# Performance work log

Measured on AMD Instinct MI355X. Metric: run time of the kernel, lower is better.

Reference implementation:

```python
import jax, jax.numpy as jnp
import numpy as np
from jax import lax

B, T = 64, 2048
ENC, DEC, ATT = 512, 1024, 128
NFILT, KSIZE = 32, 31
PAD = KSIZE // 2


def setup_inputs() -> dict:
    key = jax.random.key(0)
    ks = jax.random.split(key, 9)
    query = jax.random.normal(ks[0], (B, 1, DEC), dtype=jnp.float32)
    keys = jax.random.normal(ks[1], (B, T, ENC), dtype=jnp.float32)
    prev_weights = jax.random.uniform(ks[2], (B, T), dtype=jnp.float32)
    mask = jax.random.randint(ks[3], (B, T), 0, 2, dtype=jnp.int32)
    # params stored as [in, out] (transpose of torch Linear weight); same math
    W1 = jax.random.normal(ks[4], (ENC, ATT), dtype=jnp.float32) * (ENC ** -0.5)
    W2 = jax.random.normal(ks[5], (DEC, ATT), dtype=jnp.float32) * (DEC ** -0.5)
    V = jax.random.normal(ks[6], (ATT,), dtype=jnp.float32) * (ATT ** -0.5)
    conv_w = jax.random.normal(ks[7], (NFILT, 1, KSIZE), dtype=jnp.float32) * (KSIZE ** -0.5)
    loc_dense = jax.random.normal(ks[8], (NFILT, ATT), dtype=jnp.float32) * (NFILT ** -0.5)
    return {"query": query, "keys": keys, "prev_weights": prev_weights, "mask": mask,
            "W1": W1, "W2": W2, "V": V, "conv_w": conv_w, "loc_dense": loc_dense}


def reference(query, keys, prev_weights, mask, W1, W2, V, conv_w, loc_dense):
    proj_key = jnp.einsum('bte,ea->bta', keys, W1)          # [B,T,A]
    proj_query = jnp.einsum('bqd,da->bqa', query, W2)       # [B,1,A]
    # location conv: input [B,1,T], kernel [F,1,K], 'same' padding -> [B,F,T]
    loc_feat = lax.conv_general_dilated(prev_weights[:, None, :], conv_w,
                                        window_strides=(1,), padding=[(PAD, PAD)],
                                        dimension_numbers=('NCH', 'OIH', 'NCH'))
    proj_loc = jnp.einsum('bft,fa->bta', loc_feat, loc_dense)  # [B,T,A]
    scores = jnp.einsum('bta,a->bt', jnp.tanh(proj_key + proj_query + proj_loc), V)
    scores = jnp.where(mask == 0, -1e9, scores)
    weights = jax.nn.softmax(scores, axis=-1)                # [B,T]
    context = jnp.einsum('bt,bte->be', weights, keys)[:, None, :]  # [B,1,ENC]
    return context, weights
```

## Files before the change

### kernel.cpp

```cpp
#include <hip/hip_runtime.h>

typedef __attribute__((ext_vector_type(4))) float f32x4;
typedef __attribute__((ext_vector_type(8))) short bf16x8;

#define T_LEN 2048
#define ENC   512
#define DEC   1024
#define ATT   128
#define NB    64
#define BM    128
#define BK    32
#define NXB   (T_LEN / BM)
#define NSTEP 17

__device__ __forceinline__ unsigned short f2bf_rne(float x) {
  unsigned int u = __builtin_bit_cast(unsigned int, x);
  u += 0x7fff + ((u >> 16) & 1);
  return (unsigned short)(u >> 16);
}
__device__ __forceinline__ short f2bf_fast(float x) {
  unsigned int u = __builtin_bit_cast(unsigned int, x);
  return (short)((u + 0x8000u) >> 16);
}

__device__ __forceinline__ float fast_tanh(float x) {
  float e = __expf(2.f * x);
  return 1.f - 2.f / (e + 1.f);
}

__global__ __launch_bounds__(128) void prep(
    const float* __restrict__ query, const float* __restrict__ W2,
    const float* __restrict__ W1, const float* __restrict__ convw,
    const float* __restrict__ ldense,
    float* __restrict__ pq, unsigned short* __restrict__ Bl) {
  int bidx = blockIdx.x;
  if (bidx < NB) {
    int a = threadIdx.x;
    float acc = 0.f;
    for (int d = 0; d < DEC; ++d) acc += query[bidx * DEC + d] * W2[d * ATT + a];
    pq[bidx * ATT + a] = acc;
  } else {
    int a = bidx - NB;
    for (int k = threadIdx.x; k < NSTEP * BK; k += 128) {
      float v = 0.f;
      if (k < 512) {
        v = W1[k * ATT + a];
      } else if (k < 543) {
        int kc = k - 512;
        #pragma unroll
        for (int f = 0; f < 32; ++f) v += convw[f * 31 + kc] * ldense[f * ATT + a];
      }
      int kt = k >> 5, kk = k & 31;
      Bl[(kt * 128 + a) * BK + kk] = f2bf_rne(v);
    }
  }
}

__global__ __launch_bounds__(256, 4) void lsa_main(
    const float* __restrict__ keys, const float* __restrict__ prev,
    const int* __restrict__ mask, const unsigned short* __restrict__ Bl,
    const float* __restrict__ pq, const float* __restrict__ Vv,
    float* __restrict__ wout, float* __restrict__ dpart, float* __restrict__ cpart) {
  __shared__ unsigned short Abf[2][BM * BK];
  __shared__ float s_red[2][BM];
  __shared__ float e_vals[BM];

  const int tid = threadIdx.x;
  const int b = blockIdx.y;
  const int trow0 = blockIdx.x * BM;
  const int bid = b * NXB + blockIdx.x;

  const int lane = tid & 63;
  const int w = tid >> 6;
  const int wr = w >> 1, wc = w & 1;
  const int rsel = lane & 15, grp = lane >> 4;

  const int srow = tid >> 1;
  const int khalf = tid & 1;
  const int sq = (srow >> 1) & 3;
  const int widx0 = srow * BK + (((khalf * 2 + 0) ^ sq) * 8);
  const int widx1 = srow * BK + (((khalf * 2 + 1) ^ sq) * 8);

  const float* gA = keys + ((size_t)b * T_LEN + trow0 + srow) * ENC + khalf * 16;
  const unsigned short* gB = Bl + (size_t)(wc * 64 + rsel) * BK + grp * 8;

  const int rq = (rsel >> 1) & 3;
  const int ridx_base = (wr * 64 + rsel) * BK + ((grp ^ rq) * 8);

  f32x4 acc[4][4];
  #pragma unroll
  for (int m = 0; m < 4; ++m)
    #pragma unroll
    for (int n = 0; n < 4; ++n) acc[m][n] = (f32x4)0.f;

  {
    float a0[16];
    const f32x4* g = reinterpret_cast<const f32x4*>(gA);
    *reinterpret_cast<f32x4*>(&a0[0])  = g[0];
    *reinterpret_cast<f32x4*>(&a0[4])  = g[1];
    *reinterpret_cast<f32x4*>(&a0[8])  = g[2];
    *reinterpret_cast<f32x4*>(&a0[12]) = g[3];
    bf16x8 p0, p1;
    #pragma unroll
    for (int j = 0; j < 8; ++j) { p0[j] = f2bf_fast(a0[j]); p1[j] = f2bf_fast(a0[8 + j]); }
    *reinterpret_cast<bf16x8*>(&Abf[0][widx0]) = p0;
    *reinterpret_cast<bf16x8*>(&Abf[0][widx1]) = p1;
  }
  __syncthreads();

  #pragma unroll
  for (int t = 0; t < NSTEP; ++t) {
    bf16x8 bfr[4];
    {
      const unsigned short* gBt = gB + (size_t)t * (128 * BK);
      #pragma unroll
      for (int n = 0; n < 4; ++n)
        bfr[n] = *reinterpret_cast<const bf16x8*>(gBt + n * 16 * BK);
    }
    float anext[16];
    if (t < 15) {
      const f32x4* g = reinterpret_cast<const f32x4*>(gA + (t + 1) * BK);
      *reinterpret_cast<f32x4*>(&anext[0])  = g[0];
      *reinterpret_cast<f32x4*>(&anext[4])  = g[1];
      *reinterpret_cast<f32x4*>(&anext[8])  = g[2];
      *reinterpret_cast<f32x4*>(&anext[12]) = g[3];
    } else if (t == 15) {
      const int base = trow0 + srow + khalf * 16 - 15;
      #pragma unroll
      for (int j = 0; j < 16; ++j) {
        int kk = khalf * 16 + j;
        int pos = base + j;
        anext[j] = (kk < 31 && pos >= 0 && pos < T_LEN) ? prev[b * T_LEN + pos] : 0.f;
      }
    }
    {
      const unsigned short* Ab = Abf[t & 1];
      #pragma unroll
      for (int m = 0; m < 4; ++m) {
        bf16x8 af = *reinterpret_cast<const bf16x8*>(&Ab[ridx_base + m * 16 * BK]);
        #pragma unroll
        for (int n = 0; n < 4; ++n)
          acc[m][n] = __builtin_amdgcn_mfma_f32_16x16x32_bf16(af, bfr[n], acc[m][n], 0, 0, 0);
      }
    }
    if (t < NSTEP - 1) {
      bf16x8 p0, p1;
      #pragma unroll
      for (int j = 0; j < 8; ++j) { p0[j] = f2bf_fast(anext[j]); p1[j] = f2bf_fast(anext[8 + j]); }
      unsigned short* Aw = Abf[(t + 1) & 1];
      *reinterpret_cast<bf16x8*>(&Aw[widx0]) = p0;
      *reinterpret_cast<bf16x8*>(&Aw[widx1]) = p1;
      __syncthreads();
    }
  }

  float psum[4][4];
  #pragma unroll
  for (int m = 0; m < 4; ++m)
    #pragma unroll
    for (int i = 0; i < 4; ++i) psum[m][i] = 0.f;
  #pragma unroll
  for (int n = 0; n < 4; ++n) {
    int c = wc * 64 + n * 16 + rsel;
    float pqv = pq[b * ATT + c];
    float vv = Vv[c];
    #pragma unroll
    for (int m = 0; m < 4; ++m)
      #pragma unroll
      for (int i = 0; i < 4; ++i)
        psum[m][i] += vv * fast_tanh(acc[m][n][i] + pqv);
  }
  #pragma unroll
  for (int m = 0; m < 4; ++m)
    #pragma unroll
    for (int i = 0; i < 4; ++i) {
      float v = psum[m][i];
      v += __shfl_xor(v, 1, 64);
      v += __shfl_xor(v, 2, 64);
      v += __shfl_xor(v, 4, 64);
      v += __shfl_xor(v, 8, 64);
      psum[m][i] = v;
    }
  if (rsel == 0) {
    #pragma unroll
    for (int m = 0; m < 4; ++m)
      #pragma unroll
      for (int i = 0; i < 4; ++i)
        s_red[wc][wr * 64 + m * 16 + grp * 4 + i] = psum[m][i];
  }
  __syncthreads();

  if (tid < BM) {
    int trow = trow0 + tid;
    float s = s_red[0][tid] + s_red[1][tid];
    float e = (mask[b * T_LEN + trow] == 0) ? 0.f : __expf(s);
    wout[b * T_LEN + trow] = e;
    e_vals[tid] = e;
  }
  __syncthreads();

  if (tid < 64) {
    float v = e_vals[tid] + e_vals[tid + 64];
    #pragma unroll
    for (int off = 32; off; off >>= 1) v += __shfl_xor(v, off, 64);
    if (tid == 0) dpart[bid] = v;
  }

  float c0 = 0.f, c1 = 0.f;
  const float* krow = keys + ((size_t)b * T_LEN + trow0) * ENC;
  #pragma unroll 4
  for (int r = 0; r < BM; ++r) {
    float e = e_vals[r];
    if (e != 0.f) {
      c0 += e * krow[(size_t)r * ENC + tid];
      c1 += e * krow[(size_t)r * ENC + tid + 256];
    }
  }
  cpart[(size_t)bid * ENC + tid] = c0;
  cpart[(size_t)bid * ENC + tid + 256] = c1;
}

__global__ __launch_bounds__(256) void lsa_finalize(
    const float* __restrict__ dpart, const float* __restrict__ cpart,
    float* __restrict__ out) {
  int b = blockIdx.x, tid = threadIdx.x;
  float d = 0.f;
  #pragma unroll
  for (int i = 0; i < NXB; ++i) d += dpart[b * NXB + i];
  float inv = 1.f / d;
  for (int e = tid; e < ENC; e += 256) {
    float c = 0.f;
    #pragma unroll
    for (int i = 0; i < NXB; ++i) c += cpart[((size_t)(b * NXB + i)) * ENC + e];
    out[b * ENC + e] = c * inv;
  }
  float* wrow = out + NB * ENC + (size_t)b * T_LEN;
  for (int t = tid; t < T_LEN; t += 256) wrow[t] *= inv;
}

extern "C" void kernel_launch(void* const* d_in, const int* in_sizes, int n_in,
                              void* d_out, int out_size, void* d_ws, size_t ws_size,
                              hipStream_t stream) {
  const float* query  = (const float*)d_in[0];
  const float* keys   = (const float*)d_in[1];
  const float* prev   = (const float*)d_in[2];
  const int*   mask   = (const int*)d_in[3];
  const float* W1     = (const float*)d_in[4];
  const float* W2     = (const float*)d_in[5];
  const float* V      = (const float*)d_in[6];
  const float* convw  = (const float*)d_in[7];
  const float* ldense = (const float*)d_in[8];
  float* out = (float*)d_out;

  char* ws = (char*)d_ws;
  unsigned short* Bl = (unsigned short*)ws;
  float* pq    = (float*)(ws + 139264);
  float* dpart = (float*)(ws + 139264 + 32768);
  float* cpart = (float*)(ws + 139264 + 32768 + 4096);

  prep<<<dim3(192), dim3(128), 0, stream>>>(query, W2, W1, convw, ldense, pq, Bl);
  dim3 grid(NXB, NB);
  lsa_main<<<grid, dim3(256), 0, stream>>>(keys, prev, mask, Bl, pq, V,
                                           out + NB * ENC, dpart, cpart);
  lsa_finalize<<<dim3(NB), dim3(256), 0, stream>>>(dpart, cpart, out);
}
```

Baseline: 144.8 us.

## Stage fp32 key tiles into LDS via async global_load_lds, convert at read

The A-operand staging now uses direct global-to-LDS async copies (global_load_lds, 16 bytes per lane) of raw fp32 keys into an XOR-swizzled LDS tile, instead of loading into registers, converting to bf16 and storing. Conversion to bf16 moves to the LDS read side just before the MFMAs, and the last conv step is handled in a peeled iteration. The aim is to free registers and VALU work from the load path and overlap the global loads with compute. In exchange it doubles the LDS footprint (fp32 tiles), which may lower occupancy, and it converts each element once per wave that reads it rather than once per tile.

```diff
diff --git a/kernel.cpp b/kernel.cpp
--- a/kernel.cpp
+++ b/kernel.cpp
@@ -12,6 +12,14 @@
 #define BK    32
 #define NXB   (T_LEN / BM)
 #define NSTEP 17
+
+typedef unsigned int u32;
+typedef __attribute__((address_space(1))) const u32 gu32;
+typedef __attribute__((address_space(3))) u32 lu32;
+
+__device__ __forceinline__ void async_copy16(const float* g, float* l) {
+  __builtin_amdgcn_global_load_lds((gu32*)g, (lu32*)l, 16, 0, 0);
+}
 
 __device__ __forceinline__ unsigned short f2bf_rne(float x) {
   unsigned int u = __builtin_bit_cast(unsigned int, x);
@@ -61,7 +69,7 @@
     const int* __restrict__ mask, const unsigned short* __restrict__ Bl,
     const float* __restrict__ pq, const float* __restrict__ Vv,
     float* __restrict__ wout, float* __restrict__ dpart, float* __restrict__ cpart) {
-  __shared__ unsigned short Abf[2][BM * BK];
+  __shared__ float Abf[2][BM * BK];
   __shared__ float s_red[2][BM];
   __shared__ float e_vals[BM];
 
@@ -75,17 +83,16 @@
   const int wr = w >> 1, wc = w & 1;
   const int rsel = lane & 15, grp = lane >> 4;
 
-  const int srow = tid >> 1;
-  const int khalf = tid & 1;
-  const int sq = (srow >> 1) & 3;
-  const int widx0 = srow * BK + (((khalf * 2 + 0) ^ sq) * 8);
-  const int widx1 = srow * BK + (((khalf * 2 + 1) ^ sq) * 8);
-
-  const float* gA = keys + ((size_t)b * T_LEN + trow0 + srow) * ENC + khalf * 16;
+  const int lr = lane >> 3, cp = lane & 7;
+  const int gr = w * 32 + lr;
+  const int gc = cp ^ lr;
+  const float* gA = keys + ((size_t)b * T_LEN + trow0 + gr) * ENC + gc * 4;
+
   const unsigned short* gB = Bl + (size_t)(wc * 64 + rsel) * BK + grp * 8;
 
-  const int rq = (rsel >> 1) & 3;
-  const int ridx_base = (wr * 64 + rsel) * BK + ((grp ^ rq) * 8);
+  const int rx = rsel & 7;
+  const int ca0 = (2 * grp) ^ rx, ca1 = (2 * grp + 1) ^ rx;
+  const int arow_base = (wr * 64 + rsel) * BK;
 
   f32x4 acc[4][4];
   #pragma unroll
@@ -93,23 +100,35 @@
     #pragma unroll
     for (int n = 0; n < 4; ++n) acc[m][n] = (f32x4)0.f;
 
-  {
-    float a0[16];
-    const f32x4* g = reinterpret_cast<const f32x4*>(gA);
-    *reinterpret_cast<f32x4*>(&a0[0])  = g[0];
-    *reinterpret_cast<f32x4*>(&a0[4])  = g[1];
-    *reinterpret_cast<f32x4*>(&a0[8])  = g[2];
-    *reinterpret_cast<f32x4*>(&a0[12]) = g[3];
-    bf16x8 p0, p1;
-    #pragma unroll
-    for (int j = 0; j < 8; ++j) { p0[j] = f2bf_fast(a0[j]); p1[j] = f2bf_fast(a0[8 + j]); }
-    *reinterpret_cast<bf16x8*>(&Abf[0][widx0]) = p0;
-    *reinterpret_cast<bf16x8*>(&Abf[0][widx1]) = p1;
-  }
+  #pragma unroll
+  for (int i = 0; i < 4; ++i)
+    async_copy16(gA + (size_t)i * 8 * ENC, &Abf[0][(w * 4 + i) * 256]);
   __syncthreads();
 
-  #pragma unroll
-  for (int t = 0; t < NSTEP; ++t) {
+  for (int t = 0; t < 16; ++t) {
+    if (t < 15) {
+      const float* gt = gA + (t + 1) * BK;
+      float* dst = &Abf[(t + 1) & 1][0];
+      #pragma unroll
+      for (int i = 0; i < 4; ++i)
+        async_copy16(gt + (size_t)i * 8 * ENC, &dst[(w * 4 + i) * 256]);
+    } else {
+      const int r = tid >> 1, kh = tid & 1;
+      const int rx2 = r & 7;
+      float* dst = &Abf[0][r * BK];
+      #pragma unroll
+      for (int jc = 0; jc < 4; ++jc) {
+        int c = kh * 4 + jc;
+        f32x4 v;
+        #pragma unroll
+        for (int q = 0; q < 4; ++q) {
+          int kk = c * 4 + q;
+          int pos = trow0 + r + kk - 15;
+          v[q] = (kk < 31 && pos >= 0 && pos < T_LEN) ? prev[b * T_LEN + pos] : 0.f;
+        }
+        *reinterpret_cast<f32x4*>(&dst[(c ^ rx2) * 4]) = v;
+      }
+    }
     bf16x8 bfr[4];
     {
       const unsigned short* gBt = gB + (size_t)t * (128 * BK);
@@ -117,40 +136,39 @@
       for (int n = 0; n < 4; ++n)
         bfr[n] = *reinterpret_cast<const bf16x8*>(gBt + n * 16 * BK);
     }
-    float anext[16];
-    if (t < 15) {
-      const f32x4* g = reinterpret_cast<const f32x4*>(gA + (t + 1) * BK);
-      *reinterpret_cast<f32x4*>(&anext[0])  = g[0];
-      *reinterpret_cast<f32x4*>(&anext[4])  = g[1];
-      *reinterpret_cast<f32x4*>(&anext[8])  = g[2];
-      *reinterpret_cast<f32x4*>(&anext[12]) = g[3];
-    } else if (t == 15) {
-      const int base = trow0 + srow + khalf * 16 - 15;
-      #pragma unroll
-      for (int j = 0; j < 16; ++j) {
-        int kk = khalf * 16 + j;
-        int pos = base + j;
-        anext[j] = (kk < 31 && pos >= 0 && pos < T_LEN) ? prev[b * T_LEN + pos] : 0.f;
-      }
-    }
     {
-      const unsigned short* Ab = Abf[t & 1];
+      const float* Ab = &Abf[t & 1][0];
       #pragma unroll
       for (int m = 0; m < 4; ++m) {
-        bf16x8 af = *reinterpret_cast<const bf16x8*>(&Ab[ridx_base + m * 16 * BK]);
+        f32x4 x0 = *reinterpret_cast<const f32x4*>(&Ab[arow_base + m * 16 * BK + ca0 * 4]);
+        f32x4 x1 = *reinterpret_cast<const f32x4*>(&Ab[arow_base + m * 16 * BK + ca1 * 4]);
+        bf16x8 af;
+        #pragma unroll
+        for (int j = 0; j < 4; ++j) { af[j] = f2bf_fast(x0[j]); af[4 + j] = f2bf_fast(x1[j]); }
         #pragma unroll
         for (int n = 0; n < 4; ++n)
           acc[m][n] = __builtin_amdgcn_mfma_f32_16x16x32_bf16(af, bfr[n], acc[m][n], 0, 0, 0);
       }
     }
-    if (t < NSTEP - 1) {
-      bf16x8 p0, p1;
-      #pragma unroll
-      for (int j = 0; j < 8; ++j) { p0[j] = f2bf_fast(anext[j]); p1[j] = f2bf_fast(anext[8 + j]); }
-      unsigned short* Aw = Abf[(t + 1) & 1];
-      *reinterpret_cast<bf16x8*>(&Aw[widx0]) = p0;
-      *reinterpret_cast<bf16x8*>(&Aw[widx1]) = p1;
-      __syncthreads();
+    __syncthreads();
+  }
+  {
+    bf16x8 bfr[4];
+    const unsigned short* gBt = gB + (size_t)16 * (128 * BK);
+    #pragma unroll
+    for (int n = 0; n < 4; ++n)
+      bfr[n] = *reinterpret_cast<const bf16x8*>(gBt + n * 16 * BK);
+    const float* Ab = &Abf[0][0];
+    #pragma unroll
+    for (int m = 0; m < 4; ++m) {
+      f32x4 x0 = *reinterpret_cast<const f32x4*>(&Ab[arow_base + m * 16 * BK + ca0 * 4]);
+      f32x4 x1 = *reinterpret_cast<const f32x4*>(&Ab[arow_base + m * 16 * BK + ca1 * 4]);
+      bf16x8 af;
+      #pragma unroll
+      for (int j = 0; j < 4; ++j) { af[j] = f2bf_fast(x0[j]); af[4 + j] = f2bf_fast(x1[j]); }
+      #pragma unroll
+      for (int n = 0; n < 4; ++n)
+        acc[m][n] = __builtin_amdgcn_mfma_f32_16x16x32_bf16(af, bfr[n], acc[m][n], 0, 0, 0);
     }
   }
 
```

Result: faster. 135.5 us (-6.4%).
